# Kernel tuning notes

Hardware: AMD Instinct MI355X
Metric: run time of the kernel (lower is better)

Reference implementation:

```python
import jax, jax.numpy as jnp
import numpy as np

IN_SHAPE = (128, 128, 128)   # (d, w, h)
RES_SCALE = 1.5
SCAN_RANGE = 11.0
PROJ_NUM = 4
SPACING = np.array([1.0, 1.0, 1.0])
OUT_SHAPE = (256, 256)
BATCH = 2


def _make_grids():
    # Faithful numpy port of proj_layer._project_grid_multi (precomputed buffers).
    d, w, h = IN_SHAPE
    p = PROJ_NUM
    half = SCAN_RANGE / 2.0
    poses = np.zeros((p, 3))
    poses[:, 1] = 3.0
    poses[:, 0] = np.tan(np.linspace(-half, half, p) / 180.0 * np.pi) * 3.0
    poses[:, 2] = np.linspace(-0.2, 0.2, p)
    emi = poses * w                                  # emitter positions, (p,3)
    res_d, res_h = int(d * RES_SCALE), int(h * RES_SCALE)
    Nvec = np.array([0.0, 1.0, 0.0])
    P0 = np.linspace(0, w - 1, w)[:, None] * np.array([[0.0, 1.0, 0.0]])  # (w,3)
    lin_x = np.linspace(-res_d / 2, res_d / 2 - 1, res_d)
    lin_y = np.linspace(-res_h / 2, res_h / 2 - 1, res_h)
    gx, gy = np.meshgrid(lin_x, lin_y, indexing='ij')
    I = np.stack([gx, np.zeros_like(gx), gy], axis=-1)   # (rd,rh,3) detector plane
    I = I[None] - emi[:, None, None, :]                  # (p,rd,rh,3) ray dirs
    dxr = I / I[..., 1:2]
    In = I / np.linalg.norm(I, axis=3, keepdims=True)
    dxr = np.linalg.norm(dxr * SPACING[None, None, None, :], axis=3)  # (p,rd,rh) step length
    inv_IN = 1.0 / (In @ Nvec)                           # (p,rd,rh)
    PN = (P0[None] - emi[:, None, :]) @ Nvec             # (p,w)
    T = inv_IN[..., None] * PN[:, None, None, :]         # (p,rd,rh,w) ray params
    grid = In[..., None, :] * T[..., None] + emi[:, None, None, None, :]  # (p,rd,rh,w,3)
    gn = np.empty_like(grid)
    gn[..., 0] = grid[..., 0] / d * 2.0
    gn[..., 1] = grid[..., 1] / w * 2.0 - 1.0
    gn[..., 2] = grid[..., 2] / h * 2.0
    gn = gn[..., ::-1]  # torch.flip(grid, [4]) -> grid_sample (x,y,z) order
    return np.ascontiguousarray(gn).astype(np.float32), dxr.astype(np.float32)


def setup_inputs() -> dict:
    key = jax.random.key(0)
    x = jax.random.normal(key, (BATCH,) + IN_SHAPE, dtype=jnp.float32)
    g, dxr = _make_grids()
    return {"x": x, "grids": jnp.asarray(g), "dx": jnp.asarray(dxr)}


def _trilinear_gather(vol, coords):
    # vol: (b, D, H, W); coords: (N,3) normalized [-1,1], (x,y,z) -> (W,H,D)
    # F.grid_sample(mode='bilinear', padding_mode='zeros', align_corners=True)
    b, D, H, W = vol.shape
    ix = (coords[:, 0] + 1.0) * 0.5 * (W - 1)
    iy = (coords[:, 1] + 1.0) * 0.5 * (H - 1)
    iz = (coords[:, 2] + 1.0) * 0.5 * (D - 1)
    x0, y0, z0 = jnp.floor(ix), jnp.floor(iy), jnp.floor(iz)
    fx, fy, fz = ix - x0, iy - y0, iz - z0
    volf = vol.reshape(b, -1)
    out = jnp.zeros((b, coords.shape[0]), vol.dtype)
    for dz in (0, 1):
        wz = fz if dz else 1.0 - fz
        zi = z0 + dz
        for dy in (0, 1):
            wy = fy if dy else 1.0 - fy
            yi = y0 + dy
            for dxx in (0, 1):
                wx = fx if dxx else 1.0 - fx
                xi = x0 + dxx
                valid = ((xi >= 0) & (xi <= W - 1) & (yi >= 0) & (yi <= H - 1)
                         & (zi >= 0) & (zi <= D - 1))
                idx = ((jnp.clip(zi, 0, D - 1).astype(jnp.int32) * H
                        + jnp.clip(yi, 0, H - 1).astype(jnp.int32)) * W
                       + jnp.clip(xi, 0, W - 1).astype(jnp.int32))
                wgt = jnp.where(valid, wx * wy * wz, 0.0)
                out = out + volf[:, idx] * wgt[None, :]
    return out


def _nearest_resize(t, out_hw):
    # F.interpolate(mode='nearest'): src = floor(dst * in / out)
    b, c, H, W = t.shape
    oh, ow = out_hw
    hi = jnp.minimum((jnp.arange(oh) * H) // oh, H - 1)
    wi = jnp.minimum((jnp.arange(ow) * W) // ow, W - 1)
    return t[:, :, hi][:, :, :, wi]


def reference(x, grids, dx):
    p, rd, rh, w = grids.shape[:4]
    b = x.shape[0]
    coords = grids.reshape(-1, 3)                       # (p*rd*rh*w, 3)
    samples = _trilinear_gather(x, coords).reshape(b, p, rd, rh, w)
    x_proj = samples.sum(axis=4) * dx[None]             # ray-sum projection
    return _nearest_resize(x_proj, OUT_SHAPE)
```

## Files before the change

### kernel.cpp

```cpp
#include <hip/hip_runtime.h>
#include <hip/hip_bf16.h>

#define PNUM 4
#define RD   192
#define RH   192
#define OHH  256
#define OWW  256
#define NB   2
#define ROWS (PNUM * RD * RH)
#define VOL  (128 * 128 * 128)
#define NRDP (PNUM * RD)

typedef float        vf4 __attribute__((ext_vector_type(4)));
typedef float        vf2 __attribute__((ext_vector_type(2)));
typedef unsigned int vu2 __attribute__((ext_vector_type(2)));
typedef unsigned int vu4 __attribute__((ext_vector_type(4)));

__device__ __forceinline__ unsigned int bf16_bits(float f) {
    __hip_bfloat16 h = __float2bfloat16(f);
    return (unsigned int)__hip_bfloat16_raw(h).x;
}
__device__ __forceinline__ float hi_bits_f(unsigned int u) {
    u &= 0xffff0000u;
    return __builtin_bit_cast(float, u);
}
__device__ __forceinline__ float lo_bits_f(unsigned int u) {
    u <<= 16;
    return __builtin_bit_cast(float, u);
}
__device__ __forceinline__ vf2 unpk(unsigned int u) {
    vf2 r; r.x = lo_bits_f(u); r.y = hi_bits_f(u); return r;
}
__device__ __forceinline__ int swz(int e) { return e ^ ((e >> 4) & 7); }


__global__ __launch_bounds__(256) void ray_setup_kernel(
    const float* __restrict__ grids,
    float* __restrict__ rayp,
    float* __restrict__ zp)
{
    const int ray = (int)(blockIdx.x * 256 + threadIdx.x);
    const float* g = grids + (size_t)ray * 384;
    const vf4 L0 = *(const vf4*)g;
    const vf4 L1 = *(const vf4*)(g + 192);
    vf2 r;
    r.x = (L0.x + 1.f) * 63.5f;
    r.y = (L1.x - L0.x) * 0.9921875f;
    *(vf2*)(rayp + (size_t)ray * 2) = r;
    if ((ray % RH) == 0) {
        vf2 z;
        z.x = (L0.z + 1.f) * 63.5f;
        z.y = (L1.z - L0.z) * 0.9921875f;
        *(vf2*)(zp + (size_t)(ray / RH) * 2) = z;
    }
}

__global__ __launch_bounds__(256) void ycomb_kernel(
    const float* __restrict__ x,
    vu2* __restrict__ ycomb)
{
    const int i  = (int)(blockIdx.x * 256 + threadIdx.x);
    const int w  = i >> 14;
    const int z  = (i >> 7) & 127;
    const int xc = i & 127;

    const float WY0 = (float)w * 0.0078125f;
    const float WY1 = 1.f - WY0;
    const int   rm  = (w > 0) ? (w - 1) : 0;

    const int b0 = (z * 128 + rm) * 128;
    const int b1 = (z * 128 + w) * 128;
    const int x1 = (xc < 127) ? (xc + 1) : 127;

    const float a0 = fmaf(WY0, x[b0 + xc],       WY1 * x[b1 + xc]);
    const float a1 = fmaf(WY0, x[VOL + b0 + xc], WY1 * x[VOL + b1 + xc]);
    const float c0 = fmaf(WY0, x[b0 + x1],       WY1 * x[b1 + x1]);
    const float c1 = fmaf(WY0, x[VOL + b0 + x1], WY1 * x[VOL + b1 + x1]);

    vu2 q;
    q.x = bf16_bits(a0) | (bf16_bits(a1) << 16);
    q.y = bf16_bits(c0) | (bf16_bits(c1) << 16);
    ycomb[i] = q;
}

__global__ __launch_bounds__(256) void proj_kernel(
    const vu2*  __restrict__ ycomb,
    const float* __restrict__ rayp,
    const float* __restrict__ zp,
    float* __restrict__ part)
{
    __shared__ __align__(16) vu2 lds[2][4][2][128];

    const int orig = (int)blockIdx.x;
    const int bsw  = (orig & 7) * (3072 / 8) + (orig >> 3);
    const int rdp  = bsw % NRDP;
    const int q    = bsw / NRDP;
    const int wq   = q * 32;

    const int tid  = (int)threadIdx.x;
    const int wv   = tid >> 6;
    const int lane = tid & 63;

    const vf2 zv = *(const vf2*)(zp + (size_t)rdp * 2);

    const int  ray  = rdp * RH + wv * 64 + lane;
    const bool comp = (wv < 3);
    vf2 xp = {0.f, 0.f};
    if (comp) xp = *(const vf2*)(rayp + (size_t)ray * 2);

    auto stage_load = [&](int wb, vu4& t0, vu4& t1) {
#pragma unroll
        for (int k = 0; k < 2; ++k) {
            const int r  = 2 * wv + k;
            const int wo = r >> 1;
            const int zr = r & 1;
            const int w  = wb + wo;
            const float iz = fmaf((float)w, zv.y, zv.x);
            const int   zb = (int)floorf(iz);
            const int   zi = zr ? min(max(zb + 1, 0), 127) : min(max(zb, 0), 127);
            const vu4 t = ((const vu4*)(ycomb + ((size_t)w << 14) + (zi << 7)))[lane];
            if (k == 0) t0 = t; else t1 = t;
        }
    };
    auto stage_write = [&](int buf, const vu4& t0, const vu4& t1) {
#pragma unroll
        for (int k = 0; k < 2; ++k) {
            const int r  = 2 * wv + k;
            const int wo = r >> 1;
            const int zr = r & 1;
            const vu4 t  = k ? t1 : t0;
            vu2 a; a.x = t.x; a.y = t.y;
            vu2 b; b.x = t.z; b.y = t.w;
            lds[buf][wo][zr][swz(2 * lane)]     = a;
            lds[buf][wo][zr][swz(2 * lane + 1)] = b;
        }
    };

    vu4 t0, t1;
    stage_load(wq, t0, t1);
    stage_write(0, t0, t1);
    __syncthreads();

    vf2 acc = {0.f, 0.f};

    for (int c = 0; c < 8; ++c) {
        const int  buf = c & 1;
        const int  wb  = wq + c * 4;
        const bool pre = (c < 7);

        if (pre) stage_load(wb + 4, t0, t1);

        if (comp) {
#pragma unroll
            for (int wu = 0; wu < 4; ++wu) {
                const int   w  = wb + wu;
                const float wf = (float)w;
                const float ix = fmaf(wf, xp.y, xp.x);
                const float iz = fmaf(wf, zv.y, zv.x);

                const float xf = floorf(ix);
                const float fx = ix - xf;
                const int   xb = (int)xf;
                const int   xl = min(max(xb, 0), 126);
                const bool  inx = (xb >= 0) && (xb <= 126);
                const float WL = inx ? (1.f - fx) : ((xb == -1)  ? fx         : 0.f);
                const float WR = inx ? fx         : ((xb == 127) ? (1.f - fx) : 0.f);

                const float zf = floorf(iz);
                const float fz = iz - zf;
                const int   zb = (int)zf;
                const float WZ0 = (zb >= 0  && zb <= 127) ? (1.f - fz) : 0.f;
                const float WZ1 = (zb >= -1 && zb <= 126) ? fz         : 0.f;

                const int e = swz(xl);
                const vu2 q0 = lds[buf][wu][0][e];
                const vu2 q1 = lds[buf][wu][1][e];

                const vf2 vx0 = WL * unpk(q0.x) + WR * unpk(q0.y);
                const vf2 vx1 = WL * unpk(q1.x) + WR * unpk(q1.y);
                acc = acc + WZ0 * vx0 + WZ1 * vx1;
            }
        }

        if (pre) stage_write(buf ^ 1, t0, t1);
        __syncthreads();
    }

    if (comp) {
        part[((size_t)q * NB + 0) * ROWS + ray] = acc.x;
        part[((size_t)q * NB + 1) * ROWS + ray] = acc.y;
    }
}


__global__ __launch_bounds__(256) void proj_rays_fb_kernel(
    const float* __restrict__ x,
    const float* __restrict__ grids,
    float* __restrict__ part)
{
    const int tid  = (int)(blockIdx.x * blockDim.x + threadIdx.x);
    const int wave = tid >> 6;
    const int lane = tid & 63;
    const int wcc  = wave & 3;
    const int rr   = wave >> 2;
    const int ray  = rr * 64 + lane;

    const float* g  = grids + (size_t)ray * 384 + wcc * 96;
    const float* v0 = x;
    const float* v1 = x + VOL;

    float s0 = 0.f, s1 = 0.f;
    for (int w0 = 0; w0 < 32; w0 += 16) {
        const vf4* gc = (const vf4*)(g + w0 * 3);
        float cf[48];
#pragma unroll
        for (int i = 0; i < 12; ++i) {
            const vf4 t = gc[i];
            cf[4*i+0] = t.x; cf[4*i+1] = t.y; cf[4*i+2] = t.z; cf[4*i+3] = t.w;
        }
#pragma unroll
        for (int w = 0; w < 16; ++w) {
            const float ix = (cf[3*w+0] + 1.f) * 63.5f;
            const float iy = (cf[3*w+1] + 1.f) * 63.5f;
            const float iz = (cf[3*w+2] + 1.f) * 63.5f;
            const float x0f = floorf(ix), y0f = floorf(iy), z0f = floorf(iz);
            const float fxx = ix - x0f, fyy = iy - y0f, fzz = iz - z0f;
            const float wx0 = (x0f >= 0.f && x0f <= 127.f) ? (1.f-fxx) : 0.f;
            const float wx1 = (x0f+1.f >= 0.f && x0f+1.f <= 127.f) ? fxx : 0.f;
            const float wy0 = (y0f >= 0.f && y0f <= 127.f) ? (1.f-fyy) : 0.f;
            const float wy1 = (y0f+1.f >= 0.f && y0f+1.f <= 127.f) ? fyy : 0.f;
            const float wz0 = (z0f >= 0.f && z0f <= 127.f) ? (1.f-fzz) : 0.f;
            const float wz1 = (z0f+1.f >= 0.f && z0f+1.f <= 127.f) ? fzz : 0.f;
            const int xi0 = (int)fminf(fmaxf(x0f,0.f),127.f);
            const int xi1 = (int)fminf(fmaxf(x0f+1.f,0.f),127.f);
            const int yi0 = (int)fminf(fmaxf(y0f,0.f),127.f);
            const int yi1 = (int)fminf(fmaxf(y0f+1.f,0.f),127.f);
            const int zi0 = (int)fminf(fmaxf(z0f,0.f),127.f);
            const int zi1 = (int)fminf(fmaxf(z0f+1.f,0.f),127.f);
            const int b00 = (zi0*128+yi0)*128, b01 = (zi0*128+yi1)*128;
            const int b10 = (zi1*128+yi0)*128, b11 = (zi1*128+yi1)*128;
            const float w000 = wz0*wy0*wx0, w001 = wz0*wy0*wx1;
            const float w010 = wz0*wy1*wx0, w011 = wz0*wy1*wx1;
            const float w100 = wz1*wy0*wx0, w101 = wz1*wy0*wx1;
            const float w110 = wz1*wy1*wx0, w111 = wz1*wy1*wx1;
            s0 += w000*v0[b00+xi0] + w001*v0[b00+xi1] + w010*v0[b01+xi0] + w011*v0[b01+xi1]
                + w100*v0[b10+xi0] + w101*v0[b10+xi1] + w110*v0[b11+xi0] + w111*v0[b11+xi1];
            s1 += w000*v1[b00+xi0] + w001*v1[b00+xi1] + w010*v1[b01+xi0] + w011*v1[b01+xi1]
                + w100*v1[b10+xi0] + w101*v1[b10+xi1] + w110*v1[b11+xi0] + w111*v1[b11+xi1];
        }
    }
    part[((size_t)wcc * NB + 0) * ROWS + ray] = s0;
    part[((size_t)wcc * NB + 1) * ROWS + ray] = s1;
}


__global__ __launch_bounds__(256) void resize_reduce_kernel(
    const float* __restrict__ part,
    const float* __restrict__ dx,
    float* __restrict__ out,
    int wsplit)
{
    const int idx = (int)(blockIdx.x * blockDim.x + threadIdx.x);
    const int ow = idx & (OWW - 1);
    const int oh = (idx >> 8) & (OHH - 1);
    const int bp = idx >> 16;
    const int b  = bp >> 2;
    const int p  = bp & 3;
    const int hi = (oh * 3) >> 2;
    const int wi = (ow * 3) >> 2;
    const int ray = (p * RD + hi) * RH + wi;

    float s = 0.f;
    for (int wcc = 0; wcc < wsplit; ++wcc)
        s += part[((size_t)wcc * NB + b) * ROWS + ray];
    out[idx] = s * dx[ray];
}

extern "C" void kernel_launch(void* const* d_in, const int* in_sizes, int n_in,
                              void* d_out, int out_size, void* d_ws, size_t ws_size,
                              hipStream_t stream) {
    const float* x     = (const float*)d_in[0];
    const float* grids = (const float*)d_in[1];
    const float* dx    = (const float*)d_in[2];
    float* out = (float*)d_out;
    char*  ws  = (char*)d_ws;

    const size_t YC_B   = (size_t)VOL * 8;
    const size_t RAYP_B = (size_t)ROWS * 2 * 4;
    const size_t ZP_B   = (size_t)NRDP * 2 * 4;
    const size_t PART_B = (size_t)4 * NB * ROWS * 4;
    const size_t NEED   = YC_B + RAYP_B + ZP_B + PART_B;

    if (ws_size >= NEED) {
        vu2*   ycomb = (vu2*)ws;
        float* rayp  = (float*)(ws + YC_B);
        float* zp    = (float*)(ws + YC_B + RAYP_B);
        float* part  = (float*)(ws + YC_B + RAYP_B + ZP_B);

        ray_setup_kernel<<<ROWS / 256, 256, 0, stream>>>(grids, rayp, zp);
        ycomb_kernel    <<<VOL / 256, 256, 0, stream>>>(x, ycomb);
        proj_kernel     <<<4 * NRDP, 256, 0, stream>>>(ycomb, rayp, zp, part);
        resize_reduce_kernel<<<(NB * PNUM * OHH * OWW) / 256, 256, 0, stream>>>(part, dx, out, 4);
    } else {
        float* part = (float*)ws;
        proj_rays_fb_kernel<<<ROWS * 4 / 256, 256, 0, stream>>>(x, grids, part);
        resize_reduce_kernel<<<(NB * PNUM * OHH * OWW) / 256, 256, 0, stream>>>(part, dx, out, 4);
    }
}
```

Measured before the change: 309.3 us.

## Fuse y/z interpolation into projection staging and drop the bf16 precombined volume

```diff
diff --git a/kernel.cpp b/kernel.cpp
--- a/kernel.cpp
+++ b/kernel.cpp
@@ -13,24 +13,7 @@
 
 typedef float        vf4 __attribute__((ext_vector_type(4)));
 typedef float        vf2 __attribute__((ext_vector_type(2)));
-typedef unsigned int vu2 __attribute__((ext_vector_type(2)));
-typedef unsigned int vu4 __attribute__((ext_vector_type(4)));
-
-__device__ __forceinline__ unsigned int bf16_bits(float f) {
-    __hip_bfloat16 h = __float2bfloat16(f);
-    return (unsigned int)__hip_bfloat16_raw(h).x;
-}
-__device__ __forceinline__ float hi_bits_f(unsigned int u) {
-    u &= 0xffff0000u;
-    return __builtin_bit_cast(float, u);
-}
-__device__ __forceinline__ float lo_bits_f(unsigned int u) {
-    u <<= 16;
-    return __builtin_bit_cast(float, u);
-}
-__device__ __forceinline__ vf2 unpk(unsigned int u) {
-    vf2 r; r.x = lo_bits_f(u); r.y = hi_bits_f(u); return r;
-}
+
 __device__ __forceinline__ int swz(int e) { return e ^ ((e >> 4) & 7); }
 
 
@@ -55,41 +38,13 @@
     }
 }
 
-__global__ __launch_bounds__(256) void ycomb_kernel(
+__global__ __launch_bounds__(256) void proj_kernel(
     const float* __restrict__ x,
-    vu2* __restrict__ ycomb)
-{
-    const int i  = (int)(blockIdx.x * 256 + threadIdx.x);
-    const int w  = i >> 14;
-    const int z  = (i >> 7) & 127;
-    const int xc = i & 127;
-
-    const float WY0 = (float)w * 0.0078125f;
-    const float WY1 = 1.f - WY0;
-    const int   rm  = (w > 0) ? (w - 1) : 0;
-
-    const int b0 = (z * 128 + rm) * 128;
-    const int b1 = (z * 128 + w) * 128;
-    const int x1 = (xc < 127) ? (xc + 1) : 127;
-
-    const float a0 = fmaf(WY0, x[b0 + xc],       WY1 * x[b1 + xc]);
-    const float a1 = fmaf(WY0, x[VOL + b0 + xc], WY1 * x[VOL + b1 + xc]);
-    const float c0 = fmaf(WY0, x[b0 + x1],       WY1 * x[b1 + x1]);
-    const float c1 = fmaf(WY0, x[VOL + b0 + x1], WY1 * x[VOL + b1 + x1]);
-
-    vu2 q;
-    q.x = bf16_bits(a0) | (bf16_bits(a1) << 16);
-    q.y = bf16_bits(c0) | (bf16_bits(c1) << 16);
-    ycomb[i] = q;
-}
-
-__global__ __launch_bounds__(256) void proj_kernel(
-    const vu2*  __restrict__ ycomb,
     const float* __restrict__ rayp,
     const float* __restrict__ zp,
     float* __restrict__ part)
 {
-    __shared__ __align__(16) vu2 lds[2][4][2][128];
+    __shared__ __align__(16) vf2 lds[2][4][128];
 
     const int orig = (int)blockIdx.x;
     const int bsw  = (orig & 7) * (3072 / 8) + (orig >> 3);
@@ -108,37 +63,48 @@
     vf2 xp = {0.f, 0.f};
     if (comp) xp = *(const vf2*)(rayp + (size_t)ray * 2);
 
-    auto stage_load = [&](int wb, vu4& t0, vu4& t1) {
-#pragma unroll
-        for (int k = 0; k < 2; ++k) {
-            const int r  = 2 * wv + k;
-            const int wo = r >> 1;
-            const int zr = r & 1;
-            const int w  = wb + wo;
-            const float iz = fmaf((float)w, zv.y, zv.x);
-            const int   zb = (int)floorf(iz);
-            const int   zi = zr ? min(max(zb + 1, 0), 127) : min(max(zb, 0), 127);
-            const vu4 t = ((const vu4*)(ycomb + ((size_t)w << 14) + (zi << 7)))[lane];
-            if (k == 0) t0 = t; else t1 = t;
-        }
+    vf2 r00, r01, r10, r11, s00, s01, s10, s11;
+    float WY0s = 0.f, WZ0s = 0.f, WZ1s = 0.f;
+
+    auto stage_load = [&](int wb) {
+        const int   w  = wb + wv;
+        const float iz = fmaf((float)w, zv.y, zv.x);
+        const float zf = floorf(iz);
+        const float fz = iz - zf;
+        const int   zb = (int)zf;
+        const int zi0 = min(max(zb,     0), 127);
+        const int zi1 = min(max(zb + 1, 0), 127);
+        WZ0s = (zb >= 0  && zb <= 127) ? (1.f - fz) : 0.f;
+        WZ1s = (zb >= -1 && zb <= 126) ? fz         : 0.f;
+        WY0s = (float)w * 0.0078125f;
+        const int y0 = (w > 0) ? (w - 1) : 0;
+        const int y1 = w;
+        const int j  = 2 * lane;
+        const float* base0 = x + ((size_t)zi0 * 128 + y0) * 128 + j;
+        const float* base1 = x + ((size_t)zi0 * 128 + y1) * 128 + j;
+        const float* base2 = x + ((size_t)zi1 * 128 + y0) * 128 + j;
+        const float* base3 = x + ((size_t)zi1 * 128 + y1) * 128 + j;
+        r00 = *(const vf2*)base0;         r01 = *(const vf2*)base1;
+        r10 = *(const vf2*)base2;         r11 = *(const vf2*)base3;
+        s00 = *(const vf2*)(base0 + VOL); s01 = *(const vf2*)(base1 + VOL);
+        s10 = *(const vf2*)(base2 + VOL); s11 = *(const vf2*)(base3 + VOL);
     };
-    auto stage_write = [&](int buf, const vu4& t0, const vu4& t1) {
-#pragma unroll
-        for (int k = 0; k < 2; ++k) {
-            const int r  = 2 * wv + k;
-            const int wo = r >> 1;
-            const int zr = r & 1;
-            const vu4 t  = k ? t1 : t0;
-            vu2 a; a.x = t.x; a.y = t.y;
-            vu2 b; b.x = t.z; b.y = t.w;
-            lds[buf][wo][zr][swz(2 * lane)]     = a;
-            lds[buf][wo][zr][swz(2 * lane + 1)] = b;
-        }
+    auto stage_write = [&](int buf) {
+        const float WY1s = 1.f - WY0s;
+        const vf2 a0 = WY0s * r00 + WY1s * r01;
+        const vf2 b0 = WY0s * r10 + WY1s * r11;
+        const vf2 c0 = WZ0s * a0 + WZ1s * b0;
+        const vf2 a1 = WY0s * s00 + WY1s * s01;
+        const vf2 b1 = WY0s * s10 + WY1s * s11;
+        const vf2 c1 = WZ0s * a1 + WZ1s * b1;
+        vf2 e0; e0.x = c0.x; e0.y = c1.x;
+        vf2 e1; e1.x = c0.y; e1.y = c1.y;
+        lds[buf][wv][swz(2 * lane)]     = e0;
+        lds[buf][wv][swz(2 * lane + 1)] = e1;
     };
 
-    vu4 t0, t1;
-    stage_load(wq, t0, t1);
-    stage_write(0, t0, t1);
+    stage_load(wq);
+    stage_write(0);
     __syncthreads();
 
     vf2 acc = {0.f, 0.f};
@@ -148,16 +114,13 @@
         const int  wb  = wq + c * 4;
         const bool pre = (c < 7);
 
-        if (pre) stage_load(wb + 4, t0, t1);
+        if (pre) stage_load(wb + 4);
 
         if (comp) {
 #pragma unroll
             for (int wu = 0; wu < 4; ++wu) {
-                const int   w  = wb + wu;
-                const float wf = (float)w;
+                const float wf = (float)(wb + wu);
                 const float ix = fmaf(wf, xp.y, xp.x);
-                const float iz = fmaf(wf, zv.y, zv.x);
-
                 const float xf = floorf(ix);
                 const float fx = ix - xf;
                 const int   xb = (int)xf;
@@ -166,23 +129,13 @@
                 const float WL = inx ? (1.f - fx) : ((xb == -1)  ? fx         : 0.f);
                 const float WR = inx ? fx         : ((xb == 127) ? (1.f - fx) : 0.f);
 
-                const float zf = floorf(iz);
-                const float fz = iz - zf;
-                const int   zb = (int)zf;
-                const float WZ0 = (zb >= 0  && zb <= 127) ? (1.f - fz) : 0.f;
-                const float WZ1 = (zb >= -1 && zb <= 126) ? fz         : 0.f;
-
-                const int e = swz(xl);
-                const vu2 q0 = lds[buf][wu][0][e];
-                const vu2 q1 = lds[buf][wu][1][e];
-
-                const vf2 vx0 = WL * unpk(q0.x) + WR * unpk(q0.y);
-                const vf2 vx1 = WL * unpk(q1.x) + WR * unpk(q1.y);
-                acc = acc + WZ0 * vx0 + WZ1 * vx1;
+                const vf2 c0 = lds[buf][wu][swz(xl)];
+                const vf2 c1 = lds[buf][wu][swz(xl + 1)];
+                acc = acc + WL * c0 + WR * c1;
             }
         }
 
-        if (pre) stage_write(buf ^ 1, t0, t1);
+        if (pre) stage_write(buf ^ 1);
         __syncthreads();
     }
 
@@ -285,21 +238,18 @@
     float* out = (float*)d_out;
     char*  ws  = (char*)d_ws;
 
-    const size_t YC_B   = (size_t)VOL * 8;
     const size_t RAYP_B = (size_t)ROWS * 2 * 4;
     const size_t ZP_B   = (size_t)NRDP * 2 * 4;
     const size_t PART_B = (size_t)4 * NB * ROWS * 4;
-    const size_t NEED   = YC_B + RAYP_B + ZP_B + PART_B;
+    const size_t NEED   = RAYP_B + ZP_B + PART_B;
 
     if (ws_size >= NEED) {
-        vu2*   ycomb = (vu2*)ws;
-        float* rayp  = (float*)(ws + YC_B);
-        float* zp    = (float*)(ws + YC_B + RAYP_B);
-        float* part  = (float*)(ws + YC_B + RAYP_B + ZP_B);
+        float* rayp = (float*)ws;
+        float* zp   = (float*)(ws + RAYP_B);
+        float* part = (float*)(ws + RAYP_B + ZP_B);
 
         ray_setup_kernel<<<ROWS / 256, 256, 0, stream>>>(grids, rayp, zp);
-        ycomb_kernel    <<<VOL / 256, 256, 0, stream>>>(x, ycomb);
-        proj_kernel     <<<4 * NRDP, 256, 0, stream>>>(ycomb, rayp, zp, part);
+        proj_kernel     <<<4 * NRDP, 256, 0, stream>>>(x, rayp, zp, part);
         resize_reduce_kernel<<<(NB * PNUM * OHH * OWW) / 256, 256, 0, stream>>>(part, dx, out, 4);
     } else {
         float* part = (float*)ws;
```

After: 306.7 us. About the same (-0.9%).
